# Performance work log

Hardware: AMD Instinct MI355X
Metric: run time of the kernel (lower is better)

The kernel has to match this reference:

```python
import jax, jax.numpy as jnp
import numpy as np

N_NODES = 100000
N_EDGES = 1600000
D_IN = 128
D_HID = 128
D_OUT = 128


def setup_inputs() -> dict:
    key = jax.random.key(0)
    ks = jax.random.split(key, 6)
    node_features = jax.random.normal(ks[0], (N_NODES, D_IN), dtype=jnp.float32)
    edge_index = jax.random.randint(ks[1], (2, N_EDGES), 0, N_NODES, dtype=jnp.int32)
    s1 = 1.0 / np.sqrt(D_IN)
    s2 = 1.0 / np.sqrt(D_HID)
    W1 = jax.random.normal(ks[2], (D_IN, D_HID), dtype=jnp.float32) * s1
    W2 = jax.random.normal(ks[3], (D_HID, D_HID), dtype=jnp.float32) * s2
    W3 = jax.random.normal(ks[4], (D_HID, D_OUT), dtype=jnp.float32) * s2
    b1 = jnp.zeros((D_HID,), dtype=jnp.float32)
    b2 = jnp.zeros((D_HID,), dtype=jnp.float32)
    b3 = jnp.zeros((D_OUT,), dtype=jnp.float32)
    return {"node_features": node_features, "edge_index": edge_index,
            "W1": W1, "b1": b1, "W2": W2, "b2": b2, "W3": W3, "b3": b3}


def _aggregate(x, src, dst, n_nodes):
    # mean over incoming neighbors (by dst), residual add; degree clamped to >=1
    msg = jax.ops.segment_sum(x[src], dst, num_segments=n_nodes)  # [N, D]
    deg = jax.ops.segment_sum(jnp.ones_like(dst, dtype=x.dtype), dst,
                              num_segments=n_nodes)
    deg = jnp.maximum(deg, 1.0)[:, None]
    return x + msg / deg


def reference(node_features, edge_index, W1, b1, W2, b2, W3, b3):
    n_nodes = node_features.shape[0]
    src, dst = edge_index[0], edge_index[1]
    x = _aggregate(node_features, src, dst, n_nodes)
    x = jax.nn.relu(x @ W1 + b1)
    x = _aggregate(x, src, dst, n_nodes)
    x = jax.nn.relu(x @ W2 + b2)
    x = x.mean(axis=0)  # graph readout -> [D_HID]
    return x @ W3 + b3  # [D_OUT]
```

## Files before the change

### kernel.cpp

```cpp
#include <hip/hip_runtime.h>

#define D 128
#define SLOTS 64
#define NB 391
#define BINCAP 5120
#define BATCH 2048
#define EPB 8
#define CNTSTRIDE 16
#define WPITCH 136

typedef __attribute__((ext_vector_type(8))) short short8;
typedef __attribute__((ext_vector_type(4))) float float4v;

__device__ inline unsigned short f2bf(float f) {
    union { float f; unsigned u; } a; a.f = f;
    unsigned u = a.u;
    return (unsigned short)((u + 0x7fffu + ((u >> 16) & 1u)) >> 16);
}
__device__ inline float bflo(unsigned u) {
    union { unsigned u; float f; } a; a.u = u << 16; return a.f;
}
__device__ inline float bfhi(unsigned u) {
    union { unsigned u; float f; } a; a.u = u & 0xffff0000u; return a.f;
}
__device__ inline unsigned packbf(float a, float b) {
    return (unsigned)f2bf(a) | ((unsigned)f2bf(b) << 16);
}
__device__ inline unsigned pack4fp8(float a, float b, float c, float d) {
    int t = __builtin_amdgcn_cvt_pk_fp8_f32(a, b, 0, false);
    t = __builtin_amdgcn_cvt_pk_fp8_f32(c, d, t, true);
    return (unsigned)t;
}
__device__ inline unsigned char pack1fp8(float a) {
    int t = __builtin_amdgcn_cvt_pk_fp8_f32(a, 0.f, 0, false);
    return (unsigned char)(t & 0xff);
}


__global__ __launch_bounds__(256) void k_part(const int* __restrict__ src,
                                              const int* __restrict__ dst, int nE,
                                              int* __restrict__ gcnt, int* __restrict__ bins) {
    __shared__ int hist[512];
    __shared__ int scan[512];
    __shared__ int base[NB];
    __shared__ int stage[BATCH];
    __shared__ int gofs[BATCH];
    int tid = threadIdx.x;
    int start = blockIdx.x * BATCH;
    int cntB = nE - start; if (cntB > BATCH) cntB = BATCH;
    if (cntB <= 0) return;

    hist[tid] = 0; hist[tid + 256] = 0;
    __syncthreads();

    int b[EPB], r[EPB], v[EPB];
    #pragma unroll
    for (int i = 0; i < EPB; ++i) {
        int e = start + i * 256 + tid;
        if (e < nE) {
            int d = dst[e];
            b[i] = d >> 8;
            v[i] = (src[e] << 8) | (d & 255);
            r[i] = atomicAdd(&hist[b[i]], 1);
        } else b[i] = -1;
    }
    __syncthreads();

    scan[tid] = hist[tid]; scan[tid + 256] = hist[tid + 256];
    __syncthreads();
    #pragma unroll
    for (int off = 1; off < 512; off <<= 1) {
        int v0 = (tid >= off) ? scan[tid - off] : 0;
        int v1 = (tid + 256 >= off) ? scan[tid + 256 - off] : 0;
        __syncthreads();
        scan[tid] += v0; scan[tid + 256] += v1;
        __syncthreads();
    }
    if (tid < 256 && tid < NB) base[tid] = atomicAdd(&gcnt[tid * CNTSTRIDE], hist[tid]);
    if (tid + 256 < NB) base[tid + 256] = atomicAdd(&gcnt[(tid + 256) * CNTSTRIDE], hist[tid + 256]);
    __syncthreads();

    #pragma unroll
    for (int i = 0; i < EPB; ++i) {
        if (b[i] >= 0) {
            int p = scan[b[i]] - hist[b[i]] + r[i];
            int o = base[b[i]] + r[i];
            stage[p] = v[i];
            gofs[p] = (o < BINCAP) ? (b[i] * BINCAP + o) : -1;
        }
    }
    __syncthreads();

    #pragma unroll
    for (int i = 0; i < EPB; ++i) {
        int p = i * 256 + tid;
        if (p < cntB) {
            int g = gofs[p];
            if (g >= 0) bins[g] = stage[p];
        }
    }
}


__global__ __launch_bounds__(256) void k_scatter2(const int* __restrict__ gcnt,
                                                  const int* __restrict__ bins,
                                                  int* __restrict__ slots,
                                                  int* __restrict__ deg, int n, int nAll) {
    __shared__ int slotsL[128 * SLOTS];
    __shared__ int cntL[128];
    int tid = threadIdx.x;
    int bin = blockIdx.x >> 1;
    int half = blockIdx.x & 1;
    if (tid < 128) cntL[tid] = 0;
    __syncthreads();

    int c = gcnt[bin * CNTSTRIDE]; if (c > BINCAP) c = BINCAP;
    const int* eb = bins + (size_t)bin * BINCAP;
    for (int i = tid; i < c; i += 256) {
        int v = eb[i];
        int dl = v & 255;
        if ((dl >> 7) == half) {
            int p = atomicAdd(&cntL[dl & 127], 1);
            if (p < SLOTS) slotsL[(dl & 127) * SLOTS + p] = v >> 8;
        }
    }
    __syncthreads();

    int node0 = bin * 256 + half * 128;
    int remNodes = n - node0;
    if (remNodes > 128) remNodes = 128;
    if (remNodes < 0) remNodes = 0;

    if (tid < remNodes) {
        int dg = cntL[tid]; if (dg > SLOTS) dg = SLOTS;
        int dgr = (dg + 3) & ~3;
        for (int p = dg; p < dgr; ++p) slotsL[tid * SLOTS + p] = nAll;
        deg[node0 + tid] = dg;
    }
    __syncthreads();

    uint4* gout = reinterpret_cast<uint4*>(slots + (size_t)node0 * SLOTS);
    const uint4* lin = reinterpret_cast<const uint4*>(slotsL);
    int nv = remNodes * SLOTS / 4;
    for (int i = tid; i < nv; i += 256) gout[i] = lin[i];
}


__global__ void k_convert(const float* __restrict__ x, unsigned short* __restrict__ y16,
                          unsigned char* __restrict__ y8, int n4) {
    int i = blockIdx.x * 256 + threadIdx.x;
    if (i >= n4 + 32) return;
    uint2 o; unsigned o8;
    if (i < n4) {
        float4 v = reinterpret_cast<const float4*>(x)[i];
        o.x = packbf(v.x, v.y);
        o.y = packbf(v.z, v.w);
        o8 = pack4fp8(v.x, v.y, v.z, v.w);
    } else {
        o.x = 0; o.y = 0; o8 = 0;
    }
    reinterpret_cast<uint2*>(y16)[i] = o;
    reinterpret_cast<unsigned*>(y8)[i] = o8;
}


__global__ void k_agg(const unsigned short* __restrict__ Xin16,
                      const unsigned char* __restrict__ Xin8,
                      unsigned short* __restrict__ Xout,
                      const int* __restrict__ deg, const int* __restrict__ slots, int n) {
    int t = blockIdx.x * 256 + threadIdx.x;
    int node = t >> 4;
    int lane = t & 15;
    if (node >= n) return;
    int dg = deg[node];
    int cnt4 = (dg + 3) & ~3;
    float acc[8] = {0.f, 0.f, 0.f, 0.f, 0.f, 0.f, 0.f, 0.f};
    const int* sl = slots + (size_t)node * SLOTS;
    for (int j = 0; j < cnt4; j += 4) {
        int4 s4 = *reinterpret_cast<const int4*>(sl + j);
        uint2 w0 = *reinterpret_cast<const uint2*>(Xin8 + (size_t)s4.x * D + lane * 8);
        uint2 w1 = *reinterpret_cast<const uint2*>(Xin8 + (size_t)s4.y * D + lane * 8);
        uint2 w2 = *reinterpret_cast<const uint2*>(Xin8 + (size_t)s4.z * D + lane * 8);
        uint2 w3 = *reinterpret_cast<const uint2*>(Xin8 + (size_t)s4.w * D + lane * 8);
        #pragma unroll
        for (int h = 0; h < 1; ++h) {
            auto f0 = __builtin_amdgcn_cvt_pk_f32_fp8(w0.x, false);
            auto f1 = __builtin_amdgcn_cvt_pk_f32_fp8(w0.x, true);
            auto f2 = __builtin_amdgcn_cvt_pk_f32_fp8(w0.y, false);
            auto f3 = __builtin_amdgcn_cvt_pk_f32_fp8(w0.y, true);
            acc[0] += f0[0]; acc[1] += f0[1]; acc[2] += f1[0]; acc[3] += f1[1];
            acc[4] += f2[0]; acc[5] += f2[1]; acc[6] += f3[0]; acc[7] += f3[1];
            f0 = __builtin_amdgcn_cvt_pk_f32_fp8(w1.x, false);
            f1 = __builtin_amdgcn_cvt_pk_f32_fp8(w1.x, true);
            f2 = __builtin_amdgcn_cvt_pk_f32_fp8(w1.y, false);
            f3 = __builtin_amdgcn_cvt_pk_f32_fp8(w1.y, true);
            acc[0] += f0[0]; acc[1] += f0[1]; acc[2] += f1[0]; acc[3] += f1[1];
            acc[4] += f2[0]; acc[5] += f2[1]; acc[6] += f3[0]; acc[7] += f3[1];
            f0 = __builtin_amdgcn_cvt_pk_f32_fp8(w2.x, false);
            f1 = __builtin_amdgcn_cvt_pk_f32_fp8(w2.x, true);
            f2 = __builtin_amdgcn_cvt_pk_f32_fp8(w2.y, false);
            f3 = __builtin_amdgcn_cvt_pk_f32_fp8(w2.y, true);
            acc[0] += f0[0]; acc[1] += f0[1]; acc[2] += f1[0]; acc[3] += f1[1];
            acc[4] += f2[0]; acc[5] += f2[1]; acc[6] += f3[0]; acc[7] += f3[1];
            f0 = __builtin_amdgcn_cvt_pk_f32_fp8(w3.x, false);
            f1 = __builtin_amdgcn_cvt_pk_f32_fp8(w3.x, true);
            f2 = __builtin_amdgcn_cvt_pk_f32_fp8(w3.y, false);
            f3 = __builtin_amdgcn_cvt_pk_f32_fp8(w3.y, true);
            acc[0] += f0[0]; acc[1] += f0[1]; acc[2] += f1[0]; acc[3] += f1[1];
            acc[4] += f2[0]; acc[5] += f2[1]; acc[6] += f3[0]; acc[7] += f3[1];
        }
    }
    float inv = 1.0f / (float)(dg > 0 ? dg : 1);
    uint4 sv = reinterpret_cast<const uint4*>(Xin16 + (size_t)node * D)[lane];
    float o[8];
    o[0] = bflo(sv.x) + acc[0] * inv; o[1] = bfhi(sv.x) + acc[1] * inv;
    o[2] = bflo(sv.y) + acc[2] * inv; o[3] = bfhi(sv.y) + acc[3] * inv;
    o[4] = bflo(sv.z) + acc[4] * inv; o[5] = bfhi(sv.z) + acc[5] * inv;
    o[6] = bflo(sv.w) + acc[6] * inv; o[7] = bfhi(sv.w) + acc[7] * inv;
    uint4 ov;
    ov.x = packbf(o[0], o[1]); ov.y = packbf(o[2], o[3]);
    ov.z = packbf(o[4], o[5]); ov.w = packbf(o[6], o[7]);
    reinterpret_cast<uint4*>(Xout + (size_t)node * D)[lane] = ov;
}


__global__ __launch_bounds__(256) void k_gemm(const unsigned short* __restrict__ X,
                                              const float* __restrict__ W,
                                              const float* __restrict__ bias,
                                              unsigned short* __restrict__ Y,
                                              unsigned char* __restrict__ Y8,
                                              float* __restrict__ colsum,
                                              int n, int mode) {
    __shared__ unsigned short Wt[128 * WPITCH];
    __shared__ float cs[128];
    int tid = threadIdx.x;
    int wave = tid >> 6, L = tid & 63;
    int m16 = L & 15, g = L >> 4;

    #pragma unroll
    for (int i = 0; i < 8; ++i) {
        int p = i * 256 + tid;
        int col = p & 127, kg = p >> 7;
        unsigned pk[4];
        #pragma unroll
        for (int h = 0; h < 4; ++h) {
            float w0 = W[(kg * 8 + 2 * h + 0) * 128 + col];
            float w1 = W[(kg * 8 + 2 * h + 1) * 128 + col];
            pk[h] = packbf(w0, w1);
        }
        *reinterpret_cast<uint4*>(&Wt[col * WPITCH + kg * 8]) =
            make_uint4(pk[0], pk[1], pk[2], pk[3]);
    }
    if (mode && tid < 128) cs[tid] = 0.f;
    __syncthreads();

    int row0 = blockIdx.x * 128 + wave * 32;
    float4v zero4 = {0.f, 0.f, 0.f, 0.f};
    float4v acc[2][8];
    #pragma unroll
    for (int rt = 0; rt < 2; ++rt)
        #pragma unroll
        for (int ct = 0; ct < 8; ++ct) acc[rt][ct] = zero4;

    #pragma unroll
    for (int q = 0; q < 4; ++q) {
        int k0 = q * 32;
        short8 a[2];
        #pragma unroll
        for (int rt = 0; rt < 2; ++rt) {
            int row = row0 + rt * 16 + m16;
            short8 af = {0, 0, 0, 0, 0, 0, 0, 0};
            if (row < n)
                af = *reinterpret_cast<const short8*>(X + (size_t)row * D + k0 + g * 8);
            a[rt] = af;
        }
        #pragma unroll
        for (int ct = 0; ct < 8; ++ct) {
            short8 b = *reinterpret_cast<const short8*>(&Wt[(ct * 16 + m16) * WPITCH + k0 + g * 8]);
            acc[0][ct] = __builtin_amdgcn_mfma_f32_16x16x32_bf16(a[0], b, acc[0][ct], 0, 0, 0);
            acc[1][ct] = __builtin_amdgcn_mfma_f32_16x16x32_bf16(a[1], b, acc[1][ct], 0, 0, 0);
        }
    }

    float bj[8];
    #pragma unroll
    for (int ct = 0; ct < 8; ++ct) bj[ct] = bias[ct * 16 + m16];

    if (mode == 0) {
        #pragma unroll
        for (int rt = 0; rt < 2; ++rt)
            #pragma unroll
            for (int i = 0; i < 4; ++i) {
                int row = row0 + rt * 16 + g * 4 + i;
                if (row < n) {
                    #pragma unroll
                    for (int ct = 0; ct < 8; ++ct) {
                        float v = fmaxf(acc[rt][ct][i] + bj[ct], 0.f);
                        Y[(size_t)row * D + ct * 16 + m16] = f2bf(v);
                        Y8[(size_t)row * D + ct * 16 + m16] = pack1fp8(v);
                    }
                }
            }
    } else {
        float csv[8] = {0.f, 0.f, 0.f, 0.f, 0.f, 0.f, 0.f, 0.f};
        #pragma unroll
        for (int rt = 0; rt < 2; ++rt)
            #pragma unroll
            for (int i = 0; i < 4; ++i) {
                int row = row0 + rt * 16 + g * 4 + i;
                if (row < n) {
                    #pragma unroll
                    for (int ct = 0; ct < 8; ++ct)
                        csv[ct] += fmaxf(acc[rt][ct][i] + bj[ct], 0.f);
                }
            }
        #pragma unroll
        for (int ct = 0; ct < 8; ++ct) atomicAdd(&cs[ct * 16 + m16], csv[ct]);
        __syncthreads();
        if (tid < 128) atomicAdd(&colsum[tid], cs[tid]);
    }
}


__global__ void k_final(const float* __restrict__ colsum, const float* __restrict__ W3,
                        const float* __restrict__ b3, float* __restrict__ out, float invN) {
    int j = threadIdx.x;
    float acc = b3[j];
    #pragma unroll 8
    for (int k = 0; k < D; ++k)
        acc += colsum[k] * invN * W3[k * D + j];
    out[j] = acc;
}


extern "C" void kernel_launch(void* const* d_in, const int* in_sizes, int n_in,
                              void* d_out, int out_size, void* d_ws, size_t ws_size,
                              hipStream_t stream) {
    const float* nf = (const float*)d_in[0];
    const int*   ei = (const int*)d_in[1];
    const float* W1 = (const float*)d_in[2];
    const float* b1 = (const float*)d_in[3];
    const float* W2 = (const float*)d_in[4];
    const float* b2 = (const float*)d_in[5];
    const float* W3 = (const float*)d_in[6];
    const float* b3 = (const float*)d_in[7];
    float* out = (float*)d_out;

    int n  = in_sizes[0] / D;
    int nE = in_sizes[1] / 2;
    const int* src = ei;
    const int* dst = ei + nE;

    int nBins = (n + 255) / 256;
    int nBatches = (nE + BATCH - 1) / BATCH;

    char* ws = (char*)d_ws;
    size_t off = 0;
    auto alloc = [&](size_t bytes) -> void* {
        off = (off + 255) & ~(size_t)255;
        void* p = ws + off;
        off += bytes;
        return p;
    };
    int* gcnt  = (int*)alloc((size_t)nBins * CNTSTRIDE * 4);
    int* bins  = (int*)alloc((size_t)nBins * BINCAP * 4);
    int* slots = (int*)alloc((size_t)nBins * 256 * SLOTS * 4);
    int* deg   = (int*)alloc((size_t)n * 4);
    unsigned short* x16 = (unsigned short*)alloc((size_t)(n + 1) * D * 2);
    unsigned char*  x8  = (unsigned char*) alloc((size_t)(n + 1) * D);
    unsigned short* t16 = (unsigned short*)alloc((size_t)n * D * 2);
    unsigned short* h16 = (unsigned short*)alloc((size_t)(n + 1) * D * 2);
    unsigned char*  h8  = (unsigned char*) alloc((size_t)(n + 1) * D);
    float* colsum = (float*)alloc(128 * 4);

    hipMemsetAsync(gcnt, 0, (size_t)nBins * CNTSTRIDE * 4, stream);
    hipMemsetAsync(colsum, 0, 128 * 4, stream);
    hipMemsetAsync(h8 + (size_t)n * D, 0, D, stream);

    int gC = (n * D / 4 + 32 + 255) / 256;
    int gA = (n * 16 + 255) / 256;
    int gG = (n + 127) / 128;

    k_part<<<nBatches, 256, 0, stream>>>(src, dst, nE, gcnt, bins);
    k_convert<<<gC, 256, 0, stream>>>(nf, x16, x8, n * D / 4);
    k_scatter2<<<nBins * 2, 256, 0, stream>>>(gcnt, bins, slots, deg, n, n);

    k_agg<<<gA, 256, 0, stream>>>(x16, x8, t16, deg, slots, n);
    k_gemm<<<gG, 256, 0, stream>>>(t16, W1, b1, h16, h8, (float*)nullptr, n, 0);
    k_agg<<<gA, 256, 0, stream>>>(h16, h8, t16, deg, slots, n);
    k_gemm<<<gG, 256, 0, stream>>>(t16, W2, b2, (unsigned short*)nullptr, (unsigned char*)nullptr, colsum, n, 1);
    k_final<<<1, 128, 0, stream>>>(colsum, W3, b3, out, 1.0f / (float)n);
}
```

Measured before the change: 291.2 us.

## Drop bf16 feature copies, read self term from fp8, fuse convert into partition

Removes the bf16 versions of the input and hidden features, so the aggregation reads the self term from the fp8 buffer already used for neighbor gathers. The gemm no longer writes a bf16 output. The convert kernel is merged into the edge-partition kernel as extra blocks, which also zero colsum and the padding row, replacing two memsets. This cuts global write and read traffic and launch count, at the cost of lower precision on the residual self term.

```diff
diff --git a/kernel.cpp b/kernel.cpp
--- a/kernel.cpp
+++ b/kernel.cpp
@@ -17,12 +17,6 @@
     unsigned u = a.u;
     return (unsigned short)((u + 0x7fffu + ((u >> 16) & 1u)) >> 16);
 }
-__device__ inline float bflo(unsigned u) {
-    union { unsigned u; float f; } a; a.u = u << 16; return a.f;
-}
-__device__ inline float bfhi(unsigned u) {
-    union { unsigned u; float f; } a; a.u = u & 0xffff0000u; return a.f;
-}
 __device__ inline unsigned packbf(float a, float b) {
     return (unsigned)f2bf(a) | ((unsigned)f2bf(b) << 16);
 }
@@ -35,17 +29,48 @@
     int t = __builtin_amdgcn_cvt_pk_fp8_f32(a, 0.f, 0, false);
     return (unsigned char)(t & 0xff);
 }
-
-
-__global__ __launch_bounds__(256) void k_part(const int* __restrict__ src,
+__device__ inline void acc8fp8(float* acc, uint2 w) {
+    auto f0 = __builtin_amdgcn_cvt_pk_f32_fp8(w.x, false);
+    auto f1 = __builtin_amdgcn_cvt_pk_f32_fp8(w.x, true);
+    auto f2 = __builtin_amdgcn_cvt_pk_f32_fp8(w.y, false);
+    auto f3 = __builtin_amdgcn_cvt_pk_f32_fp8(w.y, true);
+    acc[0] += f0[0]; acc[1] += f0[1]; acc[2] += f1[0]; acc[3] += f1[1];
+    acc[4] += f2[0]; acc[5] += f2[1]; acc[6] += f3[0]; acc[7] += f3[1];
+}
+
+
+__global__ __launch_bounds__(256) void k_head(const int* __restrict__ src,
                                               const int* __restrict__ dst, int nE,
-                                              int* __restrict__ gcnt, int* __restrict__ bins) {
+                                              int* __restrict__ gcnt, int* __restrict__ bins,
+                                              const float* __restrict__ x,
+                                              unsigned char* __restrict__ y8,
+                                              unsigned char* __restrict__ h8dummy,
+                                              float* __restrict__ colsum,
+                                              int n4, int nBatches) {
     __shared__ int hist[512];
     __shared__ int scan[512];
     __shared__ int base[NB];
     __shared__ int stage[BATCH];
     __shared__ int gofs[BATCH];
     int tid = threadIdx.x;
+
+    if (blockIdx.x >= nBatches) {
+        int cb = blockIdx.x - nBatches;
+        if (cb == 0 && tid < 128) colsum[tid] = 0.f;
+        int i = cb * 256 + tid;
+        if (i >= n4 + 32) return;
+        unsigned o8;
+        if (i < n4) {
+            float4 v = reinterpret_cast<const float4*>(x)[i];
+            o8 = pack4fp8(v.x, v.y, v.z, v.w);
+        } else {
+            o8 = 0;
+            reinterpret_cast<unsigned*>(h8dummy)[i - n4] = 0;
+        }
+        reinterpret_cast<unsigned*>(y8)[i] = o8;
+        return;
+    }
+
     int start = blockIdx.x * BATCH;
     int cntB = nE - start; if (cntB > BATCH) cntB = BATCH;
     if (cntB <= 0) return;
@@ -146,26 +171,7 @@
 }
 
 
-__global__ void k_convert(const float* __restrict__ x, unsigned short* __restrict__ y16,
-                          unsigned char* __restrict__ y8, int n4) {
-    int i = blockIdx.x * 256 + threadIdx.x;
-    if (i >= n4 + 32) return;
-    uint2 o; unsigned o8;
-    if (i < n4) {
-        float4 v = reinterpret_cast<const float4*>(x)[i];
-        o.x = packbf(v.x, v.y);
-        o.y = packbf(v.z, v.w);
-        o8 = pack4fp8(v.x, v.y, v.z, v.w);
-    } else {
-        o.x = 0; o.y = 0; o8 = 0;
-    }
-    reinterpret_cast<uint2*>(y16)[i] = o;
-    reinterpret_cast<unsigned*>(y8)[i] = o8;
-}
-
-
-__global__ void k_agg(const unsigned short* __restrict__ Xin16,
-                      const unsigned char* __restrict__ Xin8,
+__global__ void k_agg(const unsigned char* __restrict__ Xin8,
                       unsigned short* __restrict__ Xout,
                       const int* __restrict__ deg, const int* __restrict__ slots, int n) {
     int t = blockIdx.x * 256 + threadIdx.x;
@@ -182,41 +188,15 @@
         uint2 w1 = *reinterpret_cast<const uint2*>(Xin8 + (size_t)s4.y * D + lane * 8);
         uint2 w2 = *reinterpret_cast<const uint2*>(Xin8 + (size_t)s4.z * D + lane * 8);
         uint2 w3 = *reinterpret_cast<const uint2*>(Xin8 + (size_t)s4.w * D + lane * 8);
-        #pragma unroll
-        for (int h = 0; h < 1; ++h) {
-            auto f0 = __builtin_amdgcn_cvt_pk_f32_fp8(w0.x, false);
-            auto f1 = __builtin_amdgcn_cvt_pk_f32_fp8(w0.x, true);
-            auto f2 = __builtin_amdgcn_cvt_pk_f32_fp8(w0.y, false);
-            auto f3 = __builtin_amdgcn_cvt_pk_f32_fp8(w0.y, true);
-            acc[0] += f0[0]; acc[1] += f0[1]; acc[2] += f1[0]; acc[3] += f1[1];
-            acc[4] += f2[0]; acc[5] += f2[1]; acc[6] += f3[0]; acc[7] += f3[1];
-            f0 = __builtin_amdgcn_cvt_pk_f32_fp8(w1.x, false);
-            f1 = __builtin_amdgcn_cvt_pk_f32_fp8(w1.x, true);
-            f2 = __builtin_amdgcn_cvt_pk_f32_fp8(w1.y, false);
-            f3 = __builtin_amdgcn_cvt_pk_f32_fp8(w1.y, true);
-            acc[0] += f0[0]; acc[1] += f0[1]; acc[2] += f1[0]; acc[3] += f1[1];
-            acc[4] += f2[0]; acc[5] += f2[1]; acc[6] += f3[0]; acc[7] += f3[1];
-            f0 = __builtin_amdgcn_cvt_pk_f32_fp8(w2.x, false);
-            f1 = __builtin_amdgcn_cvt_pk_f32_fp8(w2.x, true);
-            f2 = __builtin_amdgcn_cvt_pk_f32_fp8(w2.y, false);
-            f3 = __builtin_amdgcn_cvt_pk_f32_fp8(w2.y, true);
-            acc[0] += f0[0]; acc[1] += f0[1]; acc[2] += f1[0]; acc[3] += f1[1];
-            acc[4] += f2[0]; acc[5] += f2[1]; acc[6] += f3[0]; acc[7] += f3[1];
-            f0 = __builtin_amdgcn_cvt_pk_f32_fp8(w3.x, false);
-            f1 = __builtin_amdgcn_cvt_pk_f32_fp8(w3.x, true);
-            f2 = __builtin_amdgcn_cvt_pk_f32_fp8(w3.y, false);
-            f3 = __builtin_amdgcn_cvt_pk_f32_fp8(w3.y, true);
-            acc[0] += f0[0]; acc[1] += f0[1]; acc[2] += f1[0]; acc[3] += f1[1];
-            acc[4] += f2[0]; acc[5] += f2[1]; acc[6] += f3[0]; acc[7] += f3[1];
-        }
+        acc8fp8(acc, w0); acc8fp8(acc, w1); acc8fp8(acc, w2); acc8fp8(acc, w3);
     }
     float inv = 1.0f / (float)(dg > 0 ? dg : 1);
-    uint4 sv = reinterpret_cast<const uint4*>(Xin16 + (size_t)node * D)[lane];
+    uint2 s8 = *reinterpret_cast<const uint2*>(Xin8 + (size_t)node * D + lane * 8);
+    float self[8] = {0.f, 0.f, 0.f, 0.f, 0.f, 0.f, 0.f, 0.f};
+    acc8fp8(self, s8);
     float o[8];
-    o[0] = bflo(sv.x) + acc[0] * inv; o[1] = bfhi(sv.x) + acc[1] * inv;
-    o[2] = bflo(sv.y) + acc[2] * inv; o[3] = bfhi(sv.y) + acc[3] * inv;
-    o[4] = bflo(sv.z) + acc[4] * inv; o[5] = bfhi(sv.z) + acc[5] * inv;
-    o[6] = bflo(sv.w) + acc[6] * inv; o[7] = bfhi(sv.w) + acc[7] * inv;
+    #pragma unroll
+    for (int k = 0; k < 8; ++k) o[k] = self[k] + acc[k] * inv;
     uint4 ov;
     ov.x = packbf(o[0], o[1]); ov.y = packbf(o[2], o[3]);
     ov.z = packbf(o[4], o[5]); ov.w = packbf(o[6], o[7]);
@@ -227,7 +207,6 @@
 __global__ __launch_bounds__(256) void k_gemm(const unsigned short* __restrict__ X,
                                               const float* __restrict__ W,
                                               const float* __restrict__ bias,
-                                              unsigned short* __restrict__ Y,
                                               unsigned char* __restrict__ Y8,
                                               float* __restrict__ colsum,
                                               int n, int mode) {
@@ -296,7 +275,6 @@
                     #pragma unroll
                     for (int ct = 0; ct < 8; ++ct) {
                         float v = fmaxf(acc[rt][ct][i] + bj[ct], 0.f);
-                        Y[(size_t)row * D + ct * 16 + m16] = f2bf(v);
                         Y8[(size_t)row * D + ct * 16 + m16] = pack1fp8(v);
                     }
                 }
@@ -353,6 +331,7 @@
 
     int nBins = (n + 255) / 256;
     int nBatches = (nE + BATCH - 1) / BATCH;
+    int n4 = n * D / 4;
 
     char* ws = (char*)d_ws;
     size_t off = 0;
@@ -366,28 +345,25 @@
     int* bins  = (int*)alloc((size_t)nBins * BINCAP * 4);
     int* slots = (int*)alloc((size_t)nBins * 256 * SLOTS * 4);
     int* deg   = (int*)alloc((size_t)n * 4);
-    unsigned short* x16 = (unsigned short*)alloc((size_t)(n + 1) * D * 2);
     unsigned char*  x8  = (unsigned char*) alloc((size_t)(n + 1) * D);
     unsigned short* t16 = (unsigned short*)alloc((size_t)n * D * 2);
-    unsigned short* h16 = (unsigned short*)alloc((size_t)(n + 1) * D * 2);
     unsigned char*  h8  = (unsigned char*) alloc((size_t)(n + 1) * D);
     float* colsum = (float*)alloc(128 * 4);
 
     hipMemsetAsync(gcnt, 0, (size_t)nBins * CNTSTRIDE * 4, stream);
-    hipMemsetAsync(colsum, 0, 128 * 4, stream);
-    hipMemsetAsync(h8 + (size_t)n * D, 0, D, stream);
-
-    int gC = (n * D / 4 + 32 + 255) / 256;
+
+    int gC = (n4 + 32 + 255) / 256;
     int gA = (n * 16 + 255) / 256;
     int gG = (n + 127) / 128;
 
-    k_part<<<nBatches, 256, 0, stream>>>(src, dst, nE, gcnt, bins);
-    k_convert<<<gC, 256, 0, stream>>>(nf, x16, x8, n * D / 4);
+    k_head<<<nBatches + gC, 256, 0, stream>>>(src, dst, nE, gcnt, bins,
+                                              nf, x8, h8 + (size_t)n * D,
+                                              colsum, n4, nBatches);
     k_scatter2<<<nBins * 2, 256, 0, stream>>>(gcnt, bins, slots, deg, n, n);
 
-    k_agg<<<gA, 256, 0, stream>>>(x16, x8, t16, deg, slots, n);
-    k_gemm<<<gG, 256, 0, stream>>>(t16, W1, b1, h16, h8, (float*)nullptr, n, 0);
-    k_agg<<<gA, 256, 0, stream>>>(h16, h8, t16, deg, slots, n);
-    k_gemm<<<gG, 256, 0, stream>>>(t16, W2, b2, (unsigned short*)nullptr, (unsigned char*)nullptr, colsum, n, 1);
+    k_agg<<<gA, 256, 0, stream>>>(x8, t16, deg, slots, n);
+    k_gemm<<<gG, 256, 0, stream>>>(t16, W1, b1, h8, (float*)nullptr, n, 0);
+    k_agg<<<gA, 256, 0, stream>>>(h8, t16, deg, slots, n);
+    k_gemm<<<gG, 256, 0, stream>>>(t16, W2, b2, (unsigned char*)nullptr, colsum, n, 1);
     k_final<<<1, 128, 0, stream>>>(colsum, W3, b3, out, 1.0f / (float)n);
 }
```

Result: faster. 275.0 us (-5.6%).
